# Kernel optimization log

Hardware: AMD Instinct MI355X
Metric: run time of the kernel (lower is better)

Reference implementation:

```python
import jax, jax.numpy as jnp
import numpy as np

COST_CLASS, COST_BBOX, COST_GIOU = 2.0, 5.0, 2.0
ALPHA, GAMMA, EPS = 0.25, 2.0, 1e-8


def box_cxcywh_to_xyxy(x):
    cx, cy, w, h = x[..., 0], x[..., 1], x[..., 2], x[..., 3]
    return jnp.stack([cx - 0.5 * w, cy - 0.5 * h, cx + 0.5 * w, cy + 0.5 * h], axis=-1)


def generalized_box_iou(b1, b2):
    # b1: [N,4], b2: [M,4] in xyxy -> [N,M]
    a1 = (b1[:, 2] - b1[:, 0]) * (b1[:, 3] - b1[:, 1])
    a2 = (b2[:, 2] - b2[:, 0]) * (b2[:, 3] - b2[:, 1])
    lt = jnp.maximum(b1[:, None, :2], b2[None, :, :2])
    rb = jnp.minimum(b1[:, None, 2:], b2[None, :, 2:])
    wh = jnp.maximum(rb - lt, 0.0)
    inter = wh[..., 0] * wh[..., 1]
    union = a1[:, None] + a2[None, :] - inter
    iou = inter / jnp.maximum(union, 1e-6)
    elt = jnp.minimum(b1[:, None, :2], b2[None, :, :2])
    erb = jnp.maximum(b1[:, None, 2:], b2[None, :, 2:])
    ewh = jnp.maximum(erb - elt, 0.0)
    encl = ewh[..., 0] * ewh[..., 1]
    return iou - (encl - union) / jnp.maximum(encl, 1e-6)


def setup_inputs() -> dict:
    key = jax.random.key(0)
    k1, k2, k3, k4 = jax.random.split(key, 4)
    bs, nq, nc, nt = 16, 900, 80, 3200
    return {
        'pred_logits': jax.random.normal(k1, (bs, nq, nc), dtype=jnp.float32),
        'pred_boxes': jax.random.uniform(k2, (bs, nq, 4), dtype=jnp.float32),
        'tgt_labels': jax.random.randint(k3, (nt,), 0, nc, dtype=jnp.int32),
        'tgt_boxes': jax.random.uniform(k4, (nt, 4), dtype=jnp.float32),
    }


def reference(pred_logits, pred_boxes, tgt_labels, tgt_boxes):
    bs, nq, nc = pred_logits.shape
    out_prob = jax.nn.sigmoid(pred_logits.reshape(bs * nq, nc))  # [N, C]
    out_bbox = pred_boxes.reshape(bs * nq, 4)                    # [N, 4]

    p = out_prob[:, tgt_labels]  # [N, M] gather by target class
    neg_cost = (1.0 - ALPHA) * p ** GAMMA * (-jnp.log(1.0 - p + EPS))
    pos_cost = ALPHA * (1.0 - p) ** GAMMA * (-jnp.log(p + EPS))
    cost_class = pos_cost - neg_cost

    # L1 cdist: [N, M]
    cost_bbox = jnp.sum(jnp.abs(out_bbox[:, None, :] - tgt_boxes[None, :, :]), axis=-1)

    cost_giou = -generalized_box_iou(box_cxcywh_to_xyxy(out_bbox), box_cxcywh_to_xyxy(tgt_boxes))

    C = COST_BBOX * cost_bbox + COST_CLASS * cost_class + COST_GIOU * cost_giou
    C = jnp.nan_to_num(C, nan=1.0)
    return C.reshape(bs, nq, -1)
```

## Files before the change

### kernel.cpp

```cpp
#include <hip/hip_runtime.h>
#include <cmath>

#define NCC   80
#define QT    8
#define BLK   256
#define VT    4
#define NT_C  3200
#define NQB_C 14400
#define CPR   (NT_C / VT)
#define NRG   (NQB_C / QT)
#define CSTR  20

typedef float f32x4 __attribute__((ext_vector_type(4)));

__device__ __forceinline__ float cls_cost(float x) {
    const float p   = 1.0f / (1.0f + __expf(-x));
    const float om  = 1.0f - p;
    const float pos = 0.25f * om * om * (-__logf(p  + 1e-8f));
    const float neg = 0.75f * p  * p  * (-__logf(om + 1e-8f));
    return 2.0f * (pos - neg) + 2.0f;
}

__global__ __launch_bounds__(BLK) void cost_fast(
    const float* __restrict__ logits,
    const float* __restrict__ pboxes,
    const int*   __restrict__ labels,
    const float* __restrict__ tboxes,
    float*       __restrict__ out)
{
    __shared__ float4 s_clsv[NCC * (CSTR / 4)];
    __shared__ float4 s_qb[2 * QT];
    float* s_cls = (float*)s_clsv;

    const int  w0   = blockIdx.x * BLK;
    const int  rg0  = w0 / CPR;
    const int  row0 = rg0 * QT;
    const bool two  = (((w0 + BLK - 1) / CPR) != rg0);

    const int w  = w0 + threadIdx.x;
    const int rg = w / CPR;
    const int c  = w - rg * CPR;
    const int j  = c * VT;
    const int g8 = (rg - rg0) * QT;

    const int4 lab4 = ((const int4*)labels)[c];
    const int labk[VT] = { lab4.x, lab4.y, lab4.z, lab4.w };
    float4 tb[VT];
    float ta[VT];
#pragma unroll
    for (int k = 0; k < VT; ++k) {
        tb[k] = ((const float4*)tboxes)[j + k];
        ta[k] = tb[k].z * tb[k].w;
    }

    {
        const int nst = (two ? 2 * QT : QT) * NCC;
        const float* src = logits + row0 * NCC;
        for (int t = threadIdx.x; t < nst; t += BLK) {
            const int ro  = t / NCC;
            const int lab = t - ro * NCC;
            s_cls[lab * CSTR + ro] = cls_cost(src[t]);
        }
    }
    const int ng = two ? 2 * QT : QT;
    if (threadIdx.x < ng) {
        s_qb[threadIdx.x] = ((const float4*)pboxes)[row0 + threadIdx.x];
    }
    __syncthreads();

    const unsigned obase = (unsigned)(rg * QT) * NT_C + (unsigned)j;

#pragma unroll
    for (int h = 0; h < 2; ++h) {
        const int qbase = g8 + h * 4;
        float4 c2v[VT];
#pragma unroll
        for (int k = 0; k < VT; ++k)
            c2v[k] = *(const float4*)&s_cls[labk[k] * CSTR + qbase];

        const unsigned offh = obase + (unsigned)h * 4u * NT_C;
#pragma unroll
        for (int q4 = 0; q4 < 4; ++q4) {
            const float4 qb = s_qb[qbase + q4];
            const float  qa = qb.z * qb.w;
            float res[VT];
#pragma unroll
            for (int k = 0; k < VT; ++k) {
                const float c2 = c2v[k][q4];
                const float d1 = qb.x - tb[k].x;
                const float d2 = qb.y - tb[k].y;
                const float d3 = qb.z - tb[k].z;
                const float d4 = qb.w - tb[k].w;
                const float sx = qb.z + tb[k].z;
                const float sy = qb.w + tb[k].w;
                const float dxr = fmaf(0.5f, sx, -fabsf(d1));
                const float dyr = fmaf(0.5f, sy, -fabsf(d2));
                const float dx  = fminf(fminf(dxr, qb.z), tb[k].z);
                const float dy  = fminf(fminf(dyr, qb.w), tb[k].w);
                const float iw  = fmaxf(dx, 0.0f);
                const float ih  = fmaxf(dy, 0.0f);
                const float inter = iw * ih;
                const float uni   = (qa + ta[k]) - inter;
                const float ew = sx - dx;
                const float eh = sy - dy;
                const float encl = ew * eh;
                const float r1 = __builtin_amdgcn_rcpf(fmaxf(uni,  1e-6f));
                const float r2 = __builtin_amdgcn_rcpf(fmaxf(encl, 1e-6f));
                const float l1 = (fabsf(d1) + fabsf(d2)) + (fabsf(d3) + fabsf(d4));
                float cc = fmaf(5.0f, l1, c2);
                cc = fmaf(-2.0f * inter, r1, cc);
                cc = fmaf(-2.0f * uni,  r2, cc);
                res[k] = cc;
            }
            f32x4 v = { res[0], res[1], res[2], res[3] };
            __builtin_nontemporal_store(
                v, (f32x4*)(out + offh + (unsigned)q4 * NT_C));
        }
    }
}

__global__ __launch_bounds__(BLK) void cost_generic(
    const float* __restrict__ logits, const float* __restrict__ pboxes,
    const int* __restrict__ labels, const float* __restrict__ tboxes,
    float* __restrict__ out, int NQB, int NT, int NC)
{
    extern __shared__ float smem[];
    float*  s_cls = smem;
    float4* s_qb  = (float4*)(smem + QT * NC);

    const int i0 = blockIdx.y * QT;
    const int j  = blockIdx.x * BLK + threadIdx.x;

    for (int t = threadIdx.x; t < QT * NC; t += BLK) {
        const int qi = i0 + t / NC;
        float v = 0.0f;
        if (qi < NQB) {
            const float x  = logits[qi * NC + (t % NC)];
            const float p  = 1.0f / (1.0f + __expf(-x));
            const float om = 1.0f - p;
            v = 0.25f * om * om * (-__logf(p + 1e-8f))
              - 0.75f * p * p * (-__logf(om + 1e-8f));
        }
        s_cls[t] = v;
    }
    if (threadIdx.x < QT) {
        const int qi = i0 + threadIdx.x;
        s_qb[threadIdx.x] = (qi < NQB) ? ((const float4*)pboxes)[qi]
                                       : make_float4(0.f, 0.f, 0.f, 0.f);
    }
    __syncthreads();
    if (j >= NT) return;

    const float4 tb = ((const float4*)tboxes)[j];
    const int   lab = labels[j];
    const float tx0 = tb.x - 0.5f * tb.z, tx1 = tb.x + 0.5f * tb.z;
    const float ty0 = tb.y - 0.5f * tb.w, ty1 = tb.y + 0.5f * tb.w;
    const float ta  = tb.z * tb.w;

#pragma unroll
    for (int q = 0; q < QT; ++q) {
        const float4 qb = s_qb[q];
        const float ccls = s_cls[q * NC + lab];
        const float l1 = fabsf(qb.x - tb.x) + fabsf(qb.y - tb.y)
                       + fabsf(qb.z - tb.z) + fabsf(qb.w - tb.w);
        const float qx0 = qb.x - 0.5f * qb.z, qx1 = qb.x + 0.5f * qb.z;
        const float qy0 = qb.y - 0.5f * qb.w, qy1 = qb.y + 0.5f * qb.w;
        const float qa  = qb.z * qb.w;
        const float ltx = fmaxf(qx0, tx0), lty = fmaxf(qy0, ty0);
        const float rbx = fminf(qx1, tx1), rby = fminf(qy1, ty1);
        const float iw = fmaxf(rbx - ltx, 0.f), ih = fmaxf(rby - lty, 0.f);
        const float inter = iw * ih;
        const float uni   = qa + ta - inter;
        const float iou   = inter * __builtin_amdgcn_rcpf(fmaxf(uni, 1e-6f));
        const float ex0 = fminf(qx0, tx0), ey0 = fminf(qy0, ty0);
        const float ex1 = fmaxf(qx1, tx1), ey1 = fmaxf(qy1, ty1);
        const float ew = fmaxf(ex1 - ex0, 0.f), eh = fmaxf(ey1 - ey0, 0.f);
        const float encl = ew * eh;
        const float giou = iou - (encl - uni) * __builtin_amdgcn_rcpf(fmaxf(encl, 1e-6f));
        float cc = 5.0f * l1 + 2.0f * ccls - 2.0f * giou;
        cc = (cc == cc) ? cc : 1.0f;
        const int qi = i0 + q;
        if (qi < NQB) out[(size_t)qi * NT + j] = cc;
    }
}

extern "C" void kernel_launch(void* const* d_in, const int* in_sizes, int n_in,
                              void* d_out, int out_size, void* d_ws, size_t ws_size,
                              hipStream_t stream) {
    const float* logits = (const float*)d_in[0];
    const float* pboxes = (const float*)d_in[1];
    const int*   labels = (const int*)d_in[2];
    const float* tboxes = (const float*)d_in[3];
    float*       out    = (float*)d_out;

    const int nqb = in_sizes[1] / 4;
    const int nt  = in_sizes[2];
    const int nc  = in_sizes[0] / nqb;

    if (nqb == NQB_C && nt == NT_C && nc == NCC) {
        const int nblk = (NRG * CPR) / BLK;
        hipLaunchKernelGGL(cost_fast, dim3(nblk), dim3(BLK), 0, stream,
                           logits, pboxes, labels, tboxes, out);
    } else {
        dim3 grid((nt + BLK - 1) / BLK, (nqb + QT - 1) / QT);
        size_t sm = QT * nc * sizeof(float) + QT * sizeof(float4);
        hipLaunchKernelGGL(cost_generic, grid, dim3(BLK), sm, stream,
                           logits, pboxes, labels, tboxes, out, nqb, nt, nc);
    }
}
```

Measured before the change: 51.84 us.

## Process three output tiles per block with software-prefetched target data

Each block now covers three consecutive 256-item tiles instead of one. This amortizes the shared-memory class-cost and query-box setup over more output. Each tile's labels and target boxes are loaded before the previous tile is computed, so global loads overlap with the ALU work and stores. The cost is more registers held per thread for the prefetched tile, and only a third as many blocks in the grid.

New measurement: 51.27 us. Within noise of the previous version (-1.1%).

```diff
diff --git a/kernel.cpp b/kernel.cpp
--- a/kernel.cpp
+++ b/kernel.cpp
@@ -9,6 +9,9 @@
 #define NQB_C 14400
 #define CPR   (NT_C / VT)
 #define NRG   (NQB_C / QT)
+#define TOTAL (NRG * CPR)
+#define NTILE 3
+#define WPB   (NTILE * BLK)
 #define CSTR  20
 
 typedef float f32x4 __attribute__((ext_vector_type(4)));
@@ -21,64 +24,48 @@
     return 2.0f * (pos - neg) + 2.0f;
 }
 
-__global__ __launch_bounds__(BLK) void cost_fast(
-    const float* __restrict__ logits,
-    const float* __restrict__ pboxes,
-    const int*   __restrict__ labels,
-    const float* __restrict__ tboxes,
-    float*       __restrict__ out)
-{
-    __shared__ float4 s_clsv[NCC * (CSTR / 4)];
-    __shared__ float4 s_qb[2 * QT];
-    float* s_cls = (float*)s_clsv;
-
-    const int  w0   = blockIdx.x * BLK;
-    const int  rg0  = w0 / CPR;
-    const int  row0 = rg0 * QT;
-    const bool two  = (((w0 + BLK - 1) / CPR) != rg0);
-
-    const int w  = w0 + threadIdx.x;
+struct TileIn {
+    int   labk[VT];
+    float4 tb[VT];
+    float  ta[VT];
+    int    g8;
+    unsigned obase;
+};
+
+__device__ __forceinline__ TileIn tile_load(
+    int w, int rg0,
+    const int* __restrict__ labels, const float* __restrict__ tboxes)
+{
+    TileIn t;
     const int rg = w / CPR;
     const int c  = w - rg * CPR;
     const int j  = c * VT;
-    const int g8 = (rg - rg0) * QT;
-
-    const int4 lab4 = ((const int4*)labels)[c];
-    const int labk[VT] = { lab4.x, lab4.y, lab4.z, lab4.w };
-    float4 tb[VT];
-    float ta[VT];
+    t.g8    = (rg - rg0) * QT;
+    t.obase = (unsigned)(rg * QT) * NT_C + (unsigned)j;
+    const int4 l4 = ((const int4*)labels)[c];
+    t.labk[0] = l4.x; t.labk[1] = l4.y; t.labk[2] = l4.z; t.labk[3] = l4.w;
 #pragma unroll
     for (int k = 0; k < VT; ++k) {
-        tb[k] = ((const float4*)tboxes)[j + k];
-        ta[k] = tb[k].z * tb[k].w;
-    }
-
-    {
-        const int nst = (two ? 2 * QT : QT) * NCC;
-        const float* src = logits + row0 * NCC;
-        for (int t = threadIdx.x; t < nst; t += BLK) {
-            const int ro  = t / NCC;
-            const int lab = t - ro * NCC;
-            s_cls[lab * CSTR + ro] = cls_cost(src[t]);
-        }
-    }
-    const int ng = two ? 2 * QT : QT;
-    if (threadIdx.x < ng) {
-        s_qb[threadIdx.x] = ((const float4*)pboxes)[row0 + threadIdx.x];
-    }
-    __syncthreads();
-
-    const unsigned obase = (unsigned)(rg * QT) * NT_C + (unsigned)j;
-
+        t.tb[k] = ((const float4*)tboxes)[j + k];
+        t.ta[k] = t.tb[k].z * t.tb[k].w;
+    }
+    return t;
+}
+
+__device__ __forceinline__ void tile_compute(
+    const TileIn& t,
+    const float* __restrict__ s_cls, const float4* __restrict__ s_qb,
+    float* __restrict__ out)
+{
 #pragma unroll
     for (int h = 0; h < 2; ++h) {
-        const int qbase = g8 + h * 4;
+        const int qbase = t.g8 + h * 4;
         float4 c2v[VT];
 #pragma unroll
         for (int k = 0; k < VT; ++k)
-            c2v[k] = *(const float4*)&s_cls[labk[k] * CSTR + qbase];
-
-        const unsigned offh = obase + (unsigned)h * 4u * NT_C;
+            c2v[k] = *(const float4*)&s_cls[t.labk[k] * CSTR + qbase];
+
+        const unsigned offh = t.obase + (unsigned)h * 4u * NT_C;
 #pragma unroll
         for (int q4 = 0; q4 < 4; ++q4) {
             const float4 qb = s_qb[qbase + q4];
@@ -87,20 +74,20 @@
 #pragma unroll
             for (int k = 0; k < VT; ++k) {
                 const float c2 = c2v[k][q4];
-                const float d1 = qb.x - tb[k].x;
-                const float d2 = qb.y - tb[k].y;
-                const float d3 = qb.z - tb[k].z;
-                const float d4 = qb.w - tb[k].w;
-                const float sx = qb.z + tb[k].z;
-                const float sy = qb.w + tb[k].w;
+                const float d1 = qb.x - t.tb[k].x;
+                const float d2 = qb.y - t.tb[k].y;
+                const float d3 = qb.z - t.tb[k].z;
+                const float d4 = qb.w - t.tb[k].w;
+                const float sx = qb.z + t.tb[k].z;
+                const float sy = qb.w + t.tb[k].w;
                 const float dxr = fmaf(0.5f, sx, -fabsf(d1));
                 const float dyr = fmaf(0.5f, sy, -fabsf(d2));
-                const float dx  = fminf(fminf(dxr, qb.z), tb[k].z);
-                const float dy  = fminf(fminf(dyr, qb.w), tb[k].w);
+                const float dx  = fminf(fminf(dxr, qb.z), t.tb[k].z);
+                const float dy  = fminf(fminf(dyr, qb.w), t.tb[k].w);
                 const float iw  = fmaxf(dx, 0.0f);
                 const float ih  = fmaxf(dy, 0.0f);
                 const float inter = iw * ih;
-                const float uni   = (qa + ta[k]) - inter;
+                const float uni   = (qa + t.ta[k]) - inter;
                 const float ew = sx - dx;
                 const float eh = sy - dy;
                 const float encl = ew * eh;
@@ -117,6 +104,46 @@
                 v, (f32x4*)(out + offh + (unsigned)q4 * NT_C));
         }
     }
+}
+
+__global__ __launch_bounds__(BLK) void cost_fast(
+    const float* __restrict__ logits,
+    const float* __restrict__ pboxes,
+    const int*   __restrict__ labels,
+    const float* __restrict__ tboxes,
+    float*       __restrict__ out)
+{
+    __shared__ float4 s_clsv[NCC * (CSTR / 4)];
+    __shared__ float4 s_qb[2 * QT];
+    float* s_cls = (float*)s_clsv;
+
+    const int  w0   = blockIdx.x * WPB;
+    const int  rg0  = w0 / CPR;
+    const int  row0 = rg0 * QT;
+    const bool two  = (((w0 + WPB - 1) / CPR) != rg0);
+
+    TileIn t1 = tile_load(w0 + threadIdx.x, rg0, labels, tboxes);
+
+    {
+        const int nst = (two ? 2 * QT : QT) * NCC;
+        const float* src = logits + row0 * NCC;
+        for (int t = threadIdx.x; t < nst; t += BLK) {
+            const int ro  = t / NCC;
+            const int lab = t - ro * NCC;
+            s_cls[lab * CSTR + ro] = cls_cost(src[t]);
+        }
+    }
+    const int ng = two ? 2 * QT : QT;
+    if (threadIdx.x < ng) {
+        s_qb[threadIdx.x] = ((const float4*)pboxes)[row0 + threadIdx.x];
+    }
+    __syncthreads();
+
+    TileIn t2 = tile_load(w0 + BLK + threadIdx.x, rg0, labels, tboxes);
+    tile_compute(t1, s_cls, s_qb, out);
+    TileIn t3 = tile_load(w0 + 2 * BLK + threadIdx.x, rg0, labels, tboxes);
+    tile_compute(t2, s_cls, s_qb, out);
+    tile_compute(t3, s_cls, s_qb, out);
 }
 
 __global__ __launch_bounds__(BLK) void cost_generic(
@@ -198,7 +225,7 @@
     const int nc  = in_sizes[0] / nqb;
 
     if (nqb == NQB_C && nt == NT_C && nc == NCC) {
-        const int nblk = (NRG * CPR) / BLK;
+        const int nblk = TOTAL / WPB;
         hipLaunchKernelGGL(cost_fast, dim3(nblk), dim3(BLK), 0, stream,
                            logits, pboxes, labels, tboxes, out);
     } else {
```
